# Optimization experiments

Hardware: AMD Instinct MI355X
Metric: run time of the kernel (lower is better)

Reference implementation:

```python
import jax, jax.numpy as jnp
import numpy as np

N_NODES = 20000
N_EDGES = 320000
NFEAT = 50
ALPHA = 0.2  # leaky relu slope
EPS = 1e-16


def _gat_head(x, src, dst, W, a, concat):
    # x: (N, Fin), W: (Fin, Fout), a: (2*Fout,)
    N = x.shape[0]
    Wh = x @ W                      # (N, Fout)
    Fout = W.shape[1]
    # edge_h @ a == Wh[src] @ a[:Fout] + Wh[dst] @ a[Fout:]
    s_src = Wh @ a[:Fout]           # (N,)
    s_dst = Wh @ a[Fout:]           # (N,)
    e = jax.nn.leaky_relu(s_src[src] + s_dst[dst], negative_slope=ALPHA)  # (E,)
    # segment softmax over incoming edges of each target node
    e_max = jax.ops.segment_max(e, dst, num_segments=N)   # (N,)
    e_exp = jnp.exp(e - e_max[dst])                         # (E,)
    e_sum = jax.ops.segment_sum(e_exp, dst, num_segments=N)
    att = e_exp / (e_sum[dst] + EPS)                        # (E,)
    msg = Wh[src] * att[:, None]                            # (E, Fout)
    h = jax.ops.segment_sum(msg, dst, num_segments=N)       # (N, Fout)
    return jax.nn.elu(h) if concat else h


def _multi_head(x, src, dst, W, a, concat):
    # W: (H, Fin, Fout), a: (H, 2*Fout) -> (H, N, Fout)
    return jax.vmap(_gat_head, in_axes=(None, None, None, 0, 0, None))(x, src, dst, W, a, concat)


def setup_inputs() -> dict:
    key = jax.random.key(0)
    ks = jax.random.split(key, 8)
    x = jax.random.normal(ks[0], (N_NODES, NFEAT), dtype=jnp.float32)
    edge_index = jax.random.randint(ks[1], (2, N_EDGES), 0, N_NODES, dtype=jnp.int64)
    s = 0.1
    W1 = jax.random.normal(ks[2], (4, NFEAT, 256), dtype=jnp.float32) * s
    a1 = jax.random.normal(ks[3], (4, 512), dtype=jnp.float32) * s
    W2 = jax.random.normal(ks[4], (4, 1024, 256), dtype=jnp.float32) * s
    a2 = jax.random.normal(ks[5], (4, 512), dtype=jnp.float32) * s
    W3 = jax.random.normal(ks[6], (6, 1024, 121), dtype=jnp.float32) * s
    a3 = jax.random.normal(ks[7], (6, 242), dtype=jnp.float32) * s
    return {"x": x, "edge_index": edge_index, "W1": W1, "a1": a1, "W2": W2, "a2": a2, "W3": W3, "a3": a3}


def reference(x, edge_index, W1, a1, W2, a2, W3, a3):
    src, dst = edge_index[0], edge_index[1]
    N = x.shape[0]
    # layer 1: 4 heads, concat -> (N, 1024), then elu
    h1 = _multi_head(x, src, dst, W1, a1, True)      # (4, N, 256)
    x1 = jnp.transpose(h1, (1, 0, 2)).reshape(N, -1)  # concat along feature dim
    x1 = jax.nn.elu(x1)
    # layer 2: 4 heads, concat + skip connection, then elu
    h2 = _multi_head(x1, src, dst, W2, a2, True)
    x2 = jnp.transpose(h2, (1, 0, 2)).reshape(N, -1)
    x2 = jax.nn.elu(x2 + x1)
    # layer 3: 6 heads, no concat-elu, mean over heads
    h3 = _multi_head(x2, src, dst, W3, a3, False)     # (6, N, 121)
    x3 = jnp.mean(h3, axis=0)
    return jax.nn.sigmoid(x3)
```

## Files before the change

kernel.cpp:

```cpp
#include <hip/hip_runtime.h>
#include <cstdint>

#define N_NODES 20000
#define N_EDGES 320000
#define ALPHA 0.2f
#define GAT_EPS 1e-16f
#define MPAD 20096
#define RBLK 157
#define RHI 20
#define SCAN_BLKS 80
#define BT_ROWS 1152

typedef __attribute__((ext_vector_type(8))) _Float16 half8;
typedef __attribute__((ext_vector_type(4))) _Float16 half4t;
typedef __attribute__((ext_vector_type(16))) float f32x16;
typedef __attribute__((ext_vector_type(2))) float f32x2;

__device__ __forceinline__ float elu1(float x) { return x > 0.f ? x : __expf(x) - 1.f; }

__device__ __forceinline__ unsigned char f2fp8(float x) {
    return (unsigned char)(__builtin_amdgcn_cvt_pk_fp8_f32(x, 0.f, 0, false) & 0xff);
}

__device__ __forceinline__ void async16(const void* g, void* l) {
    __builtin_amdgcn_global_load_lds(
        (const __attribute__((address_space(1))) unsigned int*)g,
        (__attribute__((address_space(3))) unsigned int*)l, 16, 0, 0);
}

__device__ __forceinline__ float rdlanef(float v, int j) {
    return __int_as_float(__builtin_amdgcn_readlane(__float_as_int(v), j));
}

__global__ void hist_kernel(const int* __restrict__ dst, int* __restrict__ counts, int E) {
    int e = blockIdx.x * blockDim.x + threadIdx.x;
    if (e < E) atomicAdd(&counts[dst[e]], 1);
}

__global__ void scan1_kernel(const int* __restrict__ counts, int* __restrict__ excl,
                             int* __restrict__ partial, int N) {
    __shared__ int sh[256];
    int t = threadIdx.x, b = blockIdx.x;
    int i = b * 256 + t;
    int v = (i < N) ? counts[i] : 0;
    sh[t] = v;
    __syncthreads();
    for (int d = 1; d < 256; d <<= 1) {
        int x = (t >= d) ? sh[t - d] : 0;
        __syncthreads();
        sh[t] += x;
        __syncthreads();
    }
    if (i < N) excl[i] = sh[t] - v;
    if (t == 255) partial[b] = sh[255];
}

__global__ void scan2_kernel(int* __restrict__ partial) {
    __shared__ int sh[128];
    int t = threadIdx.x;
    int v = (t < SCAN_BLKS) ? partial[t] : 0;
    sh[t] = v;
    __syncthreads();
    for (int d = 1; d < 128; d <<= 1) {
        int x = (t >= d) ? sh[t - d] : 0;
        __syncthreads();
        sh[t] += x;
        __syncthreads();
    }
    if (t < SCAN_BLKS) partial[t] = sh[t] - v;
}

__global__ void scan3_kernel(const int* __restrict__ excl, const int* __restrict__ partial,
                             int* __restrict__ rowptr, int* __restrict__ cursor, int N, int E) {
    int t = threadIdx.x, b = blockIdx.x;
    int i = b * 256 + t;
    if (i < N) {
        int v = excl[i] + partial[b];
        rowptr[i] = v;
        cursor[i] = v;
    }
    if (i == 0) rowptr[N] = E;
}

__global__ void scatter_kernel(const int* __restrict__ src, const int* __restrict__ dst,
                               int* __restrict__ cursor, int* __restrict__ esrc, int E) {
    int e = blockIdx.x * blockDim.x + threadIdx.x;
    if (e < E) {
        int p = atomicAdd(&cursor[dst[e]], 1);
        esrc[p] = src[e];
    }
}

__global__ void pack_x16(const float* __restrict__ x, _Float16* __restrict__ A) {
    int idx = blockIdx.x * 256 + threadIdx.x;
    int r = idx >> 6, c = idx & 63;
    float v = (r < N_NODES && c < 50) ? x[r * 50 + c] : 0.f;
    A[idx] = (_Float16)v;
}

__global__ void pack_bt1(const float* __restrict__ W, _Float16* __restrict__ Bt) {
    int idx = blockIdx.x * 256 + threadIdx.x;
    int c = idx >> 6, k = idx & 63;
    int h = c >> 8, f = c & 255;
    float v = (k < 50) ? W[((size_t)h * 50 + k) * 256 + f] : 0.f;
    Bt[idx] = (_Float16)v;
}

__global__ void pack_bt16(const float* __restrict__ W, _Float16* __restrict__ Bt,
                          int F, int Fpad, int Ctot) {
    int c = blockIdx.y;
    int k = blockIdx.x * blockDim.x + threadIdx.x;
    float v = 0.f;
    if (c < Ctot) {
        int h = c / Fpad, f = c - h * Fpad;
        if (f < F) v = W[(size_t)h * 1024 * F + (size_t)k * F + f];
    }
    Bt[(size_t)c * 1024 + k] = (_Float16)v;
}

__global__ __launch_bounds__(64) void wtilde_kernel(const float* __restrict__ W,
                                                    const float* __restrict__ a,
                                                    _Float16* __restrict__ BT, int Kreal,
                                                    int Kdim, int F, int H, int Nfeat) {
    int k = blockIdx.x, j = blockIdx.y;
    if (j >= 2 * H) return;
    int lane = threadIdx.x;
    int h = j < H ? j : j - H;
    int ao = j < H ? 0 : F;
    float s = 0.f;
    if (k < Kreal) {
        const float* wp = W + ((size_t)h * Kreal + k) * F;
        const float* ap = a + (size_t)h * 2 * F + ao;
        for (int f = lane; f < F; f += 64) s += wp[f] * ap[f];
    }
#pragma unroll
    for (int off = 32; off; off >>= 1) s += __shfl_down(s, off);
    if (lane == 0) BT[(size_t)(Nfeat + j) * Kdim + k] = (_Float16)s;
}

__global__ __launch_bounds__(256) void gemm_f16(const _Float16* __restrict__ A,
                                                const _Float16* __restrict__ BT,
                                                unsigned char* __restrict__ C8,
                                                float* __restrict__ SPRE,
                                                int M, int Nfeat, int ld, int Kdim, int Cblk) {
    int id = blockIdx.x;
    int xm = id & 7, q = id >> 3;
    int cb = q % Cblk, rh = q / Cblk;
    int rb = rh * 8 + xm;
    if (rb >= RBLK) return;
    __shared__ __align__(16) _Float16 sA[2][128 * 64];
    __shared__ __align__(16) _Float16 sB[2][128 * 64];
    int t = threadIdx.x;
    int row0 = rb * 128, col0 = cb * 128;
    int lane = t & 63, wave = t >> 6;
    int wm = wave >> 1, wn = wave & 1;
    int l31 = lane & 31;
    int lhi = lane >> 5;

    const _Float16* gA = A + (size_t)row0 * Kdim;
    const _Float16* gB = BT + (size_t)col0 * Kdim;

    int sR[4], sgl[4];
#pragma unroll
    for (int i = 0; i < 4; i++) {
        int m = i * 256 + t;
        sR[i] = m >> 3;
        sgl[i] = (m & 7) ^ (sR[i] & 7);
    }

    f32x16 acc[2][2] = {};

#pragma unroll
    for (int i = 0; i < 4; i++) {
        const _Float16* pa = gA + (size_t)sR[i] * Kdim + sgl[i] * 8;
        const _Float16* pb = gB + (size_t)sR[i] * Kdim + sgl[i] * 8;
        async16(pa, &sA[0][(i * 256 + t) * 8]);
        async16(pb, &sB[0][(i * 256 + t) * 8]);
    }

    int cur = 0;
    for (int k0 = 0; k0 < Kdim; k0 += 64) {
        __syncthreads();
        int nxt = k0 + 64;
        if (nxt < Kdim) {
            int nb = cur ^ 1;
#pragma unroll
            for (int i = 0; i < 4; i++) {
                const _Float16* pa = gA + (size_t)sR[i] * Kdim + nxt + sgl[i] * 8;
                const _Float16* pb = gB + (size_t)sR[i] * Kdim + nxt + sgl[i] * 8;
                async16(pa, &sA[nb][(i * 256 + t) * 8]);
                async16(pb, &sB[nb][(i * 256 + t) * 8]);
            }
        }
        const _Float16* cA = sA[cur];
        const _Float16* cB = sB[cur];
#pragma unroll
        for (int kk = 0; kk < 4; kk++) {
            int g = kk * 2 + lhi;
            half8 af[2], bf[2];
#pragma unroll
            for (int mt = 0; mt < 2; mt++) {
                int R = wm * 64 + mt * 32 + l31;
                int gp = g ^ (R & 7);
                af[mt] = *(const half8*)(cA + R * 64 + gp * 8);
            }
#pragma unroll
            for (int nt = 0; nt < 2; nt++) {
                int R = wn * 64 + nt * 32 + l31;
                int gp = g ^ (R & 7);
                bf[nt] = *(const half8*)(cB + R * 64 + gp * 8);
            }
#pragma unroll
            for (int mt = 0; mt < 2; mt++)
#pragma unroll
                for (int nt = 0; nt < 2; nt++)
                    acc[mt][nt] = __builtin_amdgcn_mfma_f32_32x32x16_f16(af[mt], bf[nt], acc[mt][nt], 0, 0, 0);
        }
        cur ^= 1;
    }

    int cb32 = col0 + wn * 64 + l31;
    int rb32 = row0 + wm * 64 + 4 * lhi;
#pragma unroll
    for (int mt = 0; mt < 2; mt++)
#pragma unroll
        for (int nt = 0; nt < 2; nt++) {
            int gc = cb32 + nt * 32;
            if (gc < Nfeat) {
#pragma unroll
                for (int r = 0; r < 16; r++) {
                    int gr = rb32 + mt * 32 + (r & 3) + 8 * (r >> 2);
                    if (gr < M) C8[(size_t)gr * ld + gc] = f2fp8(acc[mt][nt][r]);
                }
            } else if (gc < Nfeat + 12) {
                int j = gc - Nfeat;
#pragma unroll
                for (int r = 0; r < 16; r++) {
                    int gr = rb32 + mt * 32 + (r & 3) + 8 * (r >> 2);
                    if (gr < M) SPRE[(size_t)j * N_NODES + gr] = acc[mt][nt][r];
                }
            }
        }
}

__global__ __launch_bounds__(256) void attagg256_kernel(const int* __restrict__ rowptr,
                                                        const int* __restrict__ esrc,
                                                        const float* __restrict__ SPRE,
                                                        const unsigned char* __restrict__ WH8,
                                                        _Float16* __restrict__ X16,
                                                        int use_skip, int N) {
    int n = blockIdx.x;
    int h = threadIdx.x >> 6;
    int lane = threadIdx.x & 63;
    int start = rowptr[n], end = rowptr[n + 1];
    const float* ss = SPRE + (size_t)h * N;
    float sd = SPRE[(size_t)(4 + h) * N + n];

    float m = -1e30f, s = 0.f;
    int sidx = 0; float ssc = -1e30f;
    for (int e0 = start; e0 < end; e0 += 64) {
        int e = e0 + lane;
        bool act = e < end;
        int idx = act ? esrc[e] : 0;
        float sc = -1e30f;
        if (act) {
            sc = ss[idx] + sd;
            sc = sc > 0.f ? sc : ALPHA * sc;
        }
        sidx = idx; ssc = sc;
        float mn = fmaxf(m, sc);
        s = s * __expf(m - mn) + (act ? __expf(sc - mn) : 0.f);
        m = mn;
    }
#pragma unroll
    for (int off = 1; off < 64; off <<= 1) {
        float mo = __shfl_xor(m, off);
        float so = __shfl_xor(s, off);
        float mn = fmaxf(m, mo);
        s = s * __expf(m - mn) + so * __expf(mo - mn);
        m = mn;
    }
    float inv = 1.f / (s + GAT_EPS);

    const unsigned char* Wb = WH8 + h * 256 + lane * 4;
    float a0 = 0.f, a1 = 0.f, a2 = 0.f, a3 = 0.f;
    int lastStart = start + (((end - start - 1) >> 6) << 6);
    for (int e0 = start; e0 < end; e0 += 64) {
        int e = e0 + lane;
        bool act = e < end;
        int idx; float sc;
        if (e0 == lastStart) { idx = sidx; sc = ssc; }
        else {
            idx = act ? esrc[e] : 0;
            sc = -1e30f;
            if (act) {
                sc = ss[idx] + sd;
                sc = sc > 0.f ? sc : ALPHA * sc;
            }
        }
        float p = act ? __expf(sc - m) * inv : 0.f;
        int cnt = end - e0; if (cnt > 64) cnt = 64;
        int j = 0;
        for (; j + 4 <= cnt; j += 4) {
            int i0 = __builtin_amdgcn_readlane(idx, j);
            int i1 = __builtin_amdgcn_readlane(idx, j + 1);
            int i2 = __builtin_amdgcn_readlane(idx, j + 2);
            int i3 = __builtin_amdgcn_readlane(idx, j + 3);
            float p0 = rdlanef(p, j), p1 = rdlanef(p, j + 1);
            float p2 = rdlanef(p, j + 2), p3 = rdlanef(p, j + 3);
            unsigned int w0 = *(const unsigned int*)(Wb + (size_t)i0 * 1024);
            unsigned int w1 = *(const unsigned int*)(Wb + (size_t)i1 * 1024);
            unsigned int w2 = *(const unsigned int*)(Wb + (size_t)i2 * 1024);
            unsigned int w3 = *(const unsigned int*)(Wb + (size_t)i3 * 1024);
            f32x2 l0 = __builtin_amdgcn_cvt_pk_f32_fp8((int)w0, false);
            f32x2 h0v = __builtin_amdgcn_cvt_pk_f32_fp8((int)w0, true);
            f32x2 l1 = __builtin_amdgcn_cvt_pk_f32_fp8((int)w1, false);
            f32x2 h1v = __builtin_amdgcn_cvt_pk_f32_fp8((int)w1, true);
            f32x2 l2 = __builtin_amdgcn_cvt_pk_f32_fp8((int)w2, false);
            f32x2 h2v = __builtin_amdgcn_cvt_pk_f32_fp8((int)w2, true);
            f32x2 l3 = __builtin_amdgcn_cvt_pk_f32_fp8((int)w3, false);
            f32x2 h3v = __builtin_amdgcn_cvt_pk_f32_fp8((int)w3, true);
            a0 += p0 * l0.x + p1 * l1.x + p2 * l2.x + p3 * l3.x;
            a1 += p0 * l0.y + p1 * l1.y + p2 * l2.y + p3 * l3.y;
            a2 += p0 * h0v.x + p1 * h1v.x + p2 * h2v.x + p3 * h3v.x;
            a3 += p0 * h0v.y + p1 * h1v.y + p2 * h2v.y + p3 * h3v.y;
        }
        for (; j < cnt; j++) {
            int ij = __builtin_amdgcn_readlane(idx, j);
            float pj = rdlanef(p, j);
            unsigned int w = *(const unsigned int*)(Wb + (size_t)ij * 1024);
            f32x2 lo = __builtin_amdgcn_cvt_pk_f32_fp8((int)w, false);
            f32x2 hi = __builtin_amdgcn_cvt_pk_f32_fp8((int)w, true);
            a0 += pj * lo.x; a1 += pj * lo.y; a2 += pj * hi.x; a3 += pj * hi.y;
        }
    }

    size_t o = (size_t)n * 1024 + h * 256 + lane * 4;
    float v0, v1, v2, v3;
    if (use_skip) {
        half4t sk = *(const half4t*)(X16 + o);
        v0 = elu1(elu1(a0) + (float)sk.x);
        v1 = elu1(elu1(a1) + (float)sk.y);
        v2 = elu1(elu1(a2) + (float)sk.z);
        v3 = elu1(elu1(a3) + (float)sk.w);
    } else {
        v0 = elu1(elu1(a0)); v1 = elu1(elu1(a1));
        v2 = elu1(elu1(a2)); v3 = elu1(elu1(a3));
    }
    half4t r;
    r.x = (_Float16)v0; r.y = (_Float16)v1; r.z = (_Float16)v2; r.w = (_Float16)v3;
    *(half4t*)(X16 + o) = r;
}

__global__ __launch_bounds__(384) void attagg726_kernel(const int* __restrict__ rowptr,
                                                        const int* __restrict__ esrc,
                                                        const float* __restrict__ SPRE,
                                                        const unsigned char* __restrict__ WH8,
                                                        float* __restrict__ out, int N) {
    __shared__ float part[6][124];
    int n = blockIdx.x;
    int t = threadIdx.x;
    int h = t >> 6;
    int lane = t & 63;
    int start = rowptr[n], end = rowptr[n + 1];
    const float* ss = SPRE + (size_t)h * N;
    float sd = SPRE[(size_t)(6 + h) * N + n];

    float m = -1e30f, s = 0.f;
    int sidx = 0; float ssc = -1e30f;
    for (int e0 = start; e0 < end; e0 += 64) {
        int e = e0 + lane;
        bool act = e < end;
        int idx = act ? esrc[e] : 0;
        float sc = -1e30f;
        if (act) {
            sc = ss[idx] + sd;
            sc = sc > 0.f ? sc : ALPHA * sc;
        }
        sidx = idx; ssc = sc;
        float mn = fmaxf(m, sc);
        s = s * __expf(m - mn) + (act ? __expf(sc - mn) : 0.f);
        m = mn;
    }
#pragma unroll
    for (int off = 1; off < 64; off <<= 1) {
        float mo = __shfl_xor(m, off);
        float so = __shfl_xor(s, off);
        float mn = fmaxf(m, mo);
        s = s * __expf(m - mn) + so * __expf(mo - mn);
        m = mn;
    }
    float inv = 1.f / (s + GAT_EPS);

    const unsigned char* Wb = WH8 + h * 124 + 2 * lane;
    float a0 = 0.f, a1 = 0.f;
    int lastStart = start + (((end - start - 1) >> 6) << 6);
    for (int e0 = start; e0 < end; e0 += 64) {
        int e = e0 + lane;
        bool act = e < end;
        int idx; float sc;
        if (e0 == lastStart) { idx = sidx; sc = ssc; }
        else {
            idx = act ? esrc[e] : 0;
            sc = -1e30f;
            if (act) {
                sc = ss[idx] + sd;
                sc = sc > 0.f ? sc : ALPHA * sc;
            }
        }
        float p = act ? __expf(sc - m) * inv : 0.f;
        int cnt = end - e0; if (cnt > 64) cnt = 64;
        int j = 0;
        for (; j + 4 <= cnt; j += 4) {
            int i0 = __builtin_amdgcn_readlane(idx, j);
            int i1 = __builtin_amdgcn_readlane(idx, j + 1);
            int i2 = __builtin_amdgcn_readlane(idx, j + 2);
            int i3 = __builtin_amdgcn_readlane(idx, j + 3);
            float p0 = rdlanef(p, j), p1 = rdlanef(p, j + 1);
            float p2 = rdlanef(p, j + 2), p3 = rdlanef(p, j + 3);
            unsigned short w0 = *(const unsigned short*)(Wb + (size_t)i0 * 768);
            unsigned short w1 = *(const unsigned short*)(Wb + (size_t)i1 * 768);
            unsigned short w2 = *(const unsigned short*)(Wb + (size_t)i2 * 768);
            unsigned short w3 = *(const unsigned short*)(Wb + (size_t)i3 * 768);
            f32x2 f0 = __builtin_amdgcn_cvt_pk_f32_fp8((int)w0, false);
            f32x2 f1 = __builtin_amdgcn_cvt_pk_f32_fp8((int)w1, false);
            f32x2 f2 = __builtin_amdgcn_cvt_pk_f32_fp8((int)w2, false);
            f32x2 f3 = __builtin_amdgcn_cvt_pk_f32_fp8((int)w3, false);
            a0 += p0 * f0.x + p1 * f1.x + p2 * f2.x + p3 * f3.x;
            a1 += p0 * f0.y + p1 * f1.y + p2 * f2.y + p3 * f3.y;
        }
        for (; j < cnt; j++) {
            int ij = __builtin_amdgcn_readlane(idx, j);
            float pj = rdlanef(p, j);
            unsigned short w = *(const unsigned short*)(Wb + (size_t)ij * 768);
            f32x2 f = __builtin_amdgcn_cvt_pk_f32_fp8((int)w, false);
            a0 += pj * f.x; a1 += pj * f.y;
        }
    }
    if (lane < 62) {
        part[h][2 * lane]     = a0;
        part[h][2 * lane + 1] = a1;
    }
    __syncthreads();
    if (t < 121) {
        float tot = (part[0][t] + part[1][t] + part[2][t] +
                     part[3][t] + part[4][t] + part[5][t]) * (1.f / 6.f);
        out[(size_t)n * 121 + t] = 1.f / (1.f + __expf(-tot));
    }
}

extern "C" void kernel_launch(void* const* d_in, const int* in_sizes, int n_in,
                              void* d_out, int out_size, void* d_ws, size_t ws_size,
                              hipStream_t stream) {
    const float* x  = (const float*)d_in[0];
    const int*   ei = (const int*)d_in[1];
    const float* W1 = (const float*)d_in[2];
    const float* a1 = (const float*)d_in[3];
    const float* W2 = (const float*)d_in[4];
    const float* a2 = (const float*)d_in[5];
    const float* W3 = (const float*)d_in[6];
    const float* a3 = (const float*)d_in[7];
    float* out = (float*)d_out;
    const int N = N_NODES, E = N_EDGES;
    const int* src = ei;
    const int* dst = ei + E;

    char* ws = (char*)d_ws;
    size_t off = 0;
    auto alloc = [&](size_t b) { size_t o = off; off += (b + 255) & ~(size_t)255; return o; };
    _Float16* X16  = (_Float16*)(ws + alloc((size_t)MPAD * 1024 * 2));
    unsigned char* WH8 = (unsigned char*)(ws + alloc((size_t)MPAD * 1024));
    _Float16* BT16 = (_Float16*)(ws + alloc((size_t)BT_ROWS * 1024 * 2));
    _Float16* A1   = (_Float16*)(ws + alloc((size_t)MPAD * 64 * 2));
    _Float16* BT1  = (_Float16*)(ws + alloc((size_t)BT_ROWS * 64 * 2));
    float* SPRE   = (float*)(ws + alloc((size_t)12 * N * 4));
    int*   rowptr = (int*)(ws + alloc((size_t)(N + 1) * 4));
    int*   cursor = (int*)(ws + alloc((size_t)N * 4));
    int*   counts = (int*)(ws + alloc((size_t)N * 4));
    int*   excl   = (int*)(ws + alloc((size_t)N * 4));
    int*   partial= (int*)(ws + alloc((size_t)SCAN_BLKS * 4));
    int*   esrc   = (int*)(ws + alloc((size_t)E * 4));

    hipMemsetAsync(counts, 0, (size_t)N * 4, stream);
    hist_kernel<<<(E + 255) / 256, 256, 0, stream>>>(dst, counts, E);
    scan1_kernel<<<SCAN_BLKS, 256, 0, stream>>>(counts, excl, partial, N);
    scan2_kernel<<<1, 128, 0, stream>>>(partial);
    scan3_kernel<<<SCAN_BLKS, 256, 0, stream>>>(excl, partial, rowptr, cursor, N, E);
    scatter_kernel<<<(E + 255) / 256, 256, 0, stream>>>(src, dst, cursor, esrc, E);
    hipMemsetAsync(X16 + (size_t)N * 1024, 0, (size_t)(MPAD - N) * 1024 * 2, stream);

    pack_x16<<<MPAD * 64 / 256, 256, 0, stream>>>(x, A1);
    pack_bt1<<<1024 * 64 / 256, 256, 0, stream>>>(W1, BT1);
    wtilde_kernel<<<dim3(64, 8), 64, 0, stream>>>(W1, a1, BT1, 50, 64, 256, 4, 1024);
    gemm_f16<<<8 * RHI * 9, 256, 0, stream>>>(A1, BT1, WH8, SPRE, N, 1024, 1024, 64, 9);
    attagg256_kernel<<<N, 256, 0, stream>>>(rowptr, esrc, SPRE, WH8, X16, 0, N);

    pack_bt16<<<dim3(4, 1024), 256, 0, stream>>>(W2, BT16, 256, 256, 1024);
    wtilde_kernel<<<dim3(1024, 8), 64, 0, stream>>>(W2, a2, BT16, 1024, 1024, 256, 4, 1024);
    gemm_f16<<<8 * RHI * 9, 256, 0, stream>>>(X16, BT16, WH8, SPRE, N, 1024, 1024, 1024, 9);
    attagg256_kernel<<<N, 256, 0, stream>>>(rowptr, esrc, SPRE, WH8, X16, 1, N);

    pack_bt16<<<dim3(4, 744), 256, 0, stream>>>(W3, BT16, 121, 124, 744);
    wtilde_kernel<<<dim3(1024, 12), 64, 0, stream>>>(W3, a3, BT16, 1024, 1024, 121, 6, 744);
    gemm_f16<<<8 * RHI * 6, 256, 0, stream>>>(X16, BT16, WH8, SPRE, N, 744, 768, 1024, 6);
    attagg726_kernel<<<N, 384, 0, stream>>>(rowptr, esrc, SPRE, WH8, out, N);
}
```

Before: 462.5 us.

## Gather full 1KB edge rows with 16-byte loads split across waves via LDS

The attention-aggregation kernels no longer give each wave one head that reads 4 or 2 bytes per lane per edge. Each wave now takes every 4th or 6th edge and reads the whole fp8 row with one 16-byte load per lane, accumulating through packed FMAs. Per-edge probabilities and indices are shared through LDS, and the partial sums are reduced across waves in shared memory at the end. Layer 3 is padded to 128 columns per head so its rows are 768 bytes and aligned, and the score columns are placed inside the padding so the GEMM emits them there. This trades extra barriers and an LDS reduction for wider, better-coalesced gathers and one software-prefetched load in flight per wave.

```diff
diff --git a/kernel.cpp b/kernel.cpp
--- a/kernel.cpp
+++ b/kernel.cpp
@@ -28,8 +28,15 @@
         (__attribute__((address_space(3))) unsigned int*)l, 16, 0, 0);
 }
 
-__device__ __forceinline__ float rdlanef(float v, int j) {
-    return __int_as_float(__builtin_amdgcn_readlane(__float_as_int(v), j));
+__device__ __forceinline__ f32x2 pkfma(f32x2 a, f32x2 b, f32x2 c) {
+    f32x2 d;
+    asm("v_pk_fma_f32 %0, %1, %2, %3" : "=v"(d) : "v"(a), "v"(b), "v"(c));
+    return d;
+}
+
+template <bool HI>
+__device__ __forceinline__ f32x2 cvt8(unsigned int u) {
+    return __builtin_amdgcn_cvt_pk_f32_fp8((int)u, HI);
 }
 
 __global__ void hist_kernel(const int* __restrict__ dst, int* __restrict__ counts, int E) {
@@ -121,7 +128,8 @@
 __global__ __launch_bounds__(64) void wtilde_kernel(const float* __restrict__ W,
                                                     const float* __restrict__ a,
                                                     _Float16* __restrict__ BT, int Kreal,
-                                                    int Kdim, int F, int H, int Nfeat) {
+                                                    int Kdim, int F, int H, int Nfeat,
+                                                    int padmode) {
     int k = blockIdx.x, j = blockIdx.y;
     if (j >= 2 * H) return;
     int lane = threadIdx.x;
@@ -135,14 +143,18 @@
     }
 #pragma unroll
     for (int off = 32; off; off >>= 1) s += __shfl_down(s, off);
-    if (lane == 0) BT[(size_t)(Nfeat + j) * Kdim + k] = (_Float16)s;
+    if (lane == 0) {
+        int row = padmode ? (h * 128 + 121 + (j >= H ? 1 : 0)) : (Nfeat + j);
+        BT[(size_t)row * Kdim + k] = (_Float16)s;
+    }
 }
 
 __global__ __launch_bounds__(256) void gemm_f16(const _Float16* __restrict__ A,
                                                 const _Float16* __restrict__ BT,
                                                 unsigned char* __restrict__ C8,
                                                 float* __restrict__ SPRE,
-                                                int M, int Nfeat, int ld, int Kdim, int Cblk) {
+                                                int M, int Nfeat, int ld, int Kdim, int Cblk,
+                                                int l3pad) {
     int id = blockIdx.x;
     int xm = id & 7, q = id >> 3;
     int cb = q % Cblk, rh = q / Cblk;
@@ -227,12 +239,18 @@
         for (int nt = 0; nt < 2; nt++) {
             int gc = cb32 + nt * 32;
             if (gc < Nfeat) {
+                int fr = gc & 127;
+                int sj = (fr - 121) * 6 + (gc >> 7);
+                bool sp = l3pad && (fr == 121 || fr == 122);
 #pragma unroll
                 for (int r = 0; r < 16; r++) {
                     int gr = rb32 + mt * 32 + (r & 3) + 8 * (r >> 2);
-                    if (gr < M) C8[(size_t)gr * ld + gc] = f2fp8(acc[mt][nt][r]);
+                    if (gr < M) {
+                        C8[(size_t)gr * ld + gc] = f2fp8(acc[mt][nt][r]);
+                        if (sp) SPRE[(size_t)sj * N_NODES + gr] = acc[mt][nt][r];
+                    }
                 }
-            } else if (gc < Nfeat + 12) {
+            } else if (!l3pad && gc < Nfeat + 12) {
                 int j = gc - Nfeat;
 #pragma unroll
                 for (int r = 0; r < 16; r++) {
@@ -249,12 +267,16 @@
                                                         const unsigned char* __restrict__ WH8,
                                                         _Float16* __restrict__ X16,
                                                         int use_skip, int N) {
+    __shared__ float part[4 * 1024];
+    __shared__ float Pp[4][72];
+    __shared__ int Ii[64];
     int n = blockIdx.x;
-    int h = threadIdx.x >> 6;
-    int lane = threadIdx.x & 63;
+    int t = threadIdx.x;
+    int wv = t >> 6;
+    int lane = t & 63;
     int start = rowptr[n], end = rowptr[n + 1];
-    const float* ss = SPRE + (size_t)h * N;
-    float sd = SPRE[(size_t)(4 + h) * N + n];
+    const float* ss = SPRE + (size_t)wv * N;
+    float sd = SPRE[(size_t)(4 + wv) * N + n];
 
     float m = -1e30f, s = 0.f;
     int sidx = 0; float ssc = -1e30f;
@@ -282,8 +304,9 @@
     }
     float inv = 1.f / (s + GAT_EPS);
 
-    const unsigned char* Wb = WH8 + h * 256 + lane * 4;
-    float a0 = 0.f, a1 = 0.f, a2 = 0.f, a3 = 0.f;
+    int hf = lane >> 4;
+    const unsigned char* Wb = WH8 + lane * 16;
+    f32x2 acc[8] = {};
     int lastStart = start + (((end - start - 1) >> 6) << 6);
     for (int e0 = start; e0 < end; e0 += 64) {
         int e = e0 + lane;
@@ -299,43 +322,54 @@
             }
         }
         float p = act ? __expf(sc - m) * inv : 0.f;
+        __syncthreads();
+        Pp[wv][lane] = p;
+        if (wv == 0) Ii[lane] = idx;
+        __syncthreads();
         int cnt = end - e0; if (cnt > 64) cnt = 64;
-        int j = 0;
-        for (; j + 4 <= cnt; j += 4) {
-            int i0 = __builtin_amdgcn_readlane(idx, j);
-            int i1 = __builtin_amdgcn_readlane(idx, j + 1);
-            int i2 = __builtin_amdgcn_readlane(idx, j + 2);
-            int i3 = __builtin_amdgcn_readlane(idx, j + 3);
-            float p0 = rdlanef(p, j), p1 = rdlanef(p, j + 1);
-            float p2 = rdlanef(p, j + 2), p3 = rdlanef(p, j + 3);
-            unsigned int w0 = *(const unsigned int*)(Wb + (size_t)i0 * 1024);
-            unsigned int w1 = *(const unsigned int*)(Wb + (size_t)i1 * 1024);
-            unsigned int w2 = *(const unsigned int*)(Wb + (size_t)i2 * 1024);
-            unsigned int w3 = *(const unsigned int*)(Wb + (size_t)i3 * 1024);
-            f32x2 l0 = __builtin_amdgcn_cvt_pk_f32_fp8((int)w0, false);
-            f32x2 h0v = __builtin_amdgcn_cvt_pk_f32_fp8((int)w0, true);
-            f32x2 l1 = __builtin_amdgcn_cvt_pk_f32_fp8((int)w1, false);
-            f32x2 h1v = __builtin_amdgcn_cvt_pk_f32_fp8((int)w1, true);
-            f32x2 l2 = __builtin_amdgcn_cvt_pk_f32_fp8((int)w2, false);
-            f32x2 h2v = __builtin_amdgcn_cvt_pk_f32_fp8((int)w2, true);
-            f32x2 l3 = __builtin_amdgcn_cvt_pk_f32_fp8((int)w3, false);
-            f32x2 h3v = __builtin_amdgcn_cvt_pk_f32_fp8((int)w3, true);
-            a0 += p0 * l0.x + p1 * l1.x + p2 * l2.x + p3 * l3.x;
-            a1 += p0 * l0.y + p1 * l1.y + p2 * l2.y + p3 * l3.y;
-            a2 += p0 * h0v.x + p1 * h1v.x + p2 * h2v.x + p3 * h3v.x;
-            a3 += p0 * h0v.y + p1 * h1v.y + p2 * h2v.y + p3 * h3v.y;
-        }
-        for (; j < cnt; j++) {
-            int ij = __builtin_amdgcn_readlane(idx, j);
-            float pj = rdlanef(p, j);
-            unsigned int w = *(const unsigned int*)(Wb + (size_t)ij * 1024);
-            f32x2 lo = __builtin_amdgcn_cvt_pk_f32_fp8((int)w, false);
-            f32x2 hi = __builtin_amdgcn_cvt_pk_f32_fp8((int)w, true);
-            a0 += pj * lo.x; a1 += pj * lo.y; a2 += pj * hi.x; a3 += pj * hi.y;
-        }
-    }
-
-    size_t o = (size_t)n * 1024 + h * 256 + lane * 4;
+        int j = wv;
+        if (j < cnt) {
+            int ij = Ii[j];
+            float pj = Pp[hf][j];
+            uint4 w = *(const uint4*)(Wb + ((size_t)(unsigned)ij << 10));
+            for (;;) {
+                int j2 = j + 4;
+                bool more = j2 < cnt;
+                int ij2 = 0; float pj2 = 0.f; uint4 w2;
+                if (more) {
+                    ij2 = Ii[j2];
+                    pj2 = Pp[hf][j2];
+                    w2 = *(const uint4*)(Wb + ((size_t)(unsigned)ij2 << 10));
+                }
+                f32x2 pv; pv.x = pj; pv.y = pj;
+                acc[0] = pkfma(cvt8<false>(w.x), pv, acc[0]);
+                acc[1] = pkfma(cvt8<true>(w.x),  pv, acc[1]);
+                acc[2] = pkfma(cvt8<false>(w.y), pv, acc[2]);
+                acc[3] = pkfma(cvt8<true>(w.y),  pv, acc[3]);
+                acc[4] = pkfma(cvt8<false>(w.z), pv, acc[4]);
+                acc[5] = pkfma(cvt8<true>(w.z),  pv, acc[5]);
+                acc[6] = pkfma(cvt8<false>(w.w), pv, acc[6]);
+                acc[7] = pkfma(cvt8<true>(w.w),  pv, acc[7]);
+                if (!more) break;
+                j = j2; pj = pj2; w = w2;
+            }
+        }
+    }
+
+#pragma unroll
+    for (int k = 0; k < 8; k++)
+        *(f32x2*)&part[wv * 1024 + lane * 16 + 2 * k] = acc[k];
+    __syncthreads();
+    int f0 = t * 4;
+    float4 q0 = *(const float4*)&part[f0];
+    float4 q1 = *(const float4*)&part[1024 + f0];
+    float4 q2 = *(const float4*)&part[2048 + f0];
+    float4 q3 = *(const float4*)&part[3072 + f0];
+    float a0 = q0.x + q1.x + q2.x + q3.x;
+    float a1 = q0.y + q1.y + q2.y + q3.y;
+    float a2 = q0.z + q1.z + q2.z + q3.z;
+    float a3 = q0.w + q1.w + q2.w + q3.w;
+    size_t o = (size_t)n * 1024 + f0;
     float v0, v1, v2, v3;
     if (use_skip) {
         half4t sk = *(const half4t*)(X16 + o);
@@ -357,14 +391,16 @@
                                                         const float* __restrict__ SPRE,
                                                         const unsigned char* __restrict__ WH8,
                                                         float* __restrict__ out, int N) {
-    __shared__ float part[6][124];
+    __shared__ float part[6 * 768];
+    __shared__ float Pp[6][72];
+    __shared__ int Ii[64];
     int n = blockIdx.x;
     int t = threadIdx.x;
-    int h = t >> 6;
+    int wv = t >> 6;
     int lane = t & 63;
     int start = rowptr[n], end = rowptr[n + 1];
-    const float* ss = SPRE + (size_t)h * N;
-    float sd = SPRE[(size_t)(6 + h) * N + n];
+    const float* ss = SPRE + (size_t)wv * N;
+    float sd = SPRE[(size_t)(6 + wv) * N + n];
 
     float m = -1e30f, s = 0.f;
     int sidx = 0; float ssc = -1e30f;
@@ -392,8 +428,9 @@
     }
     float inv = 1.f / (s + GAT_EPS);
 
-    const unsigned char* Wb = WH8 + h * 124 + 2 * lane;
-    float a0 = 0.f, a1 = 0.f;
+    int hf = (lane < 48) ? (lane >> 3) : 0;
+    const unsigned char* Wb = WH8 + lane * 16;
+    f32x2 acc[8] = {};
     int lastStart = start + (((end - start - 1) >> 6) << 6);
     for (int e0 = start; e0 < end; e0 += 64) {
         int e = e0 + lane;
@@ -409,42 +446,58 @@
             }
         }
         float p = act ? __expf(sc - m) * inv : 0.f;
+        __syncthreads();
+        Pp[wv][lane] = p;
+        if (wv == 0) Ii[lane] = idx;
+        __syncthreads();
         int cnt = end - e0; if (cnt > 64) cnt = 64;
-        int j = 0;
-        for (; j + 4 <= cnt; j += 4) {
-            int i0 = __builtin_amdgcn_readlane(idx, j);
-            int i1 = __builtin_amdgcn_readlane(idx, j + 1);
-            int i2 = __builtin_amdgcn_readlane(idx, j + 2);
-            int i3 = __builtin_amdgcn_readlane(idx, j + 3);
-            float p0 = rdlanef(p, j), p1 = rdlanef(p, j + 1);
-            float p2 = rdlanef(p, j + 2), p3 = rdlanef(p, j + 3);
-            unsigned short w0 = *(const unsigned short*)(Wb + (size_t)i0 * 768);
-            unsigned short w1 = *(const unsigned short*)(Wb + (size_t)i1 * 768);
-            unsigned short w2 = *(const unsigned short*)(Wb + (size_t)i2 * 768);
-            unsigned short w3 = *(const unsigned short*)(Wb + (size_t)i3 * 768);
-            f32x2 f0 = __builtin_amdgcn_cvt_pk_f32_fp8((int)w0, false);
-            f32x2 f1 = __builtin_amdgcn_cvt_pk_f32_fp8((int)w1, false);
-            f32x2 f2 = __builtin_amdgcn_cvt_pk_f32_fp8((int)w2, false);
-            f32x2 f3 = __builtin_amdgcn_cvt_pk_f32_fp8((int)w3, false);
-            a0 += p0 * f0.x + p1 * f1.x + p2 * f2.x + p3 * f3.x;
-            a1 += p0 * f0.y + p1 * f1.y + p2 * f2.y + p3 * f3.y;
-        }
-        for (; j < cnt; j++) {
-            int ij = __builtin_amdgcn_readlane(idx, j);
-            float pj = rdlanef(p, j);
-            unsigned short w = *(const unsigned short*)(Wb + (size_t)ij * 768);
-            f32x2 f = __builtin_amdgcn_cvt_pk_f32_fp8((int)w, false);
-            a0 += pj * f.x; a1 += pj * f.y;
-        }
-    }
-    if (lane < 62) {
-        part[h][2 * lane]     = a0;
-        part[h][2 * lane + 1] = a1;
+        int j = wv;
+        if (j < cnt) {
+            int ij = Ii[j];
+            float pj = Pp[hf][j];
+            uint4 w = *(const uint4*)(Wb + (size_t)(unsigned)ij * 768u);
+            for (;;) {
+                int j2 = j + 6;
+                bool more = j2 < cnt;
+                int ij2 = 0; float pj2 = 0.f; uint4 w2;
+                if (more) {
+                    ij2 = Ii[j2];
+                    pj2 = Pp[hf][j2];
+                    w2 = *(const uint4*)(Wb + (size_t)(unsigned)ij2 * 768u);
+                }
+                f32x2 pv; pv.x = pj; pv.y = pj;
+                acc[0] = pkfma(cvt8<false>(w.x), pv, acc[0]);
+                acc[1] = pkfma(cvt8<true>(w.x),  pv, acc[1]);
+                acc[2] = pkfma(cvt8<false>(w.y), pv, acc[2]);
+                acc[3] = pkfma(cvt8<true>(w.y),  pv, acc[3]);
+                acc[4] = pkfma(cvt8<false>(w.z), pv, acc[4]);
+                acc[5] = pkfma(cvt8<true>(w.z),  pv, acc[5]);
+                acc[6] = pkfma(cvt8<false>(w.w), pv, acc[6]);
+                acc[7] = pkfma(cvt8<true>(w.w),  pv, acc[7]);
+                if (!more) break;
+                j = j2; pj = pj2; w = w2;
+            }
+        }
+    }
+
+    if (lane < 48) {
+#pragma unroll
+        for (int k = 0; k < 8; k++)
+            *(f32x2*)&part[wv * 768 + lane * 16 + 2 * k] = acc[k];
+    }
+    __syncthreads();
+    for (int f = t; f < 768; f += 384) {
+        float sx = 0.f;
+#pragma unroll
+        for (int w6 = 0; w6 < 6; w6++) sx += part[w6 * 768 + f];
+        part[f] = sx;
     }
     __syncthreads();
     if (t < 121) {
-        float tot = (part[0][t] + part[1][t] + part[2][t] +
-                     part[3][t] + part[4][t] + part[5][t]) * (1.f / 6.f);
+        float tot = 0.f;
+#pragma unroll
+        for (int hh = 0; hh < 6; hh++) tot += part[hh * 128 + t];
+        tot *= (1.f / 6.f);
         out[(size_t)n * 121 + t] = 1.f / (1.f + __expf(-tot));
     }
 }
@@ -491,17 +544,17 @@
 
     pack_x16<<<MPAD * 64 / 256, 256, 0, stream>>>(x, A1);
     pack_bt1<<<1024 * 64 / 256, 256, 0, stream>>>(W1, BT1);
-    wtilde_kernel<<<dim3(64, 8), 64, 0, stream>>>(W1, a1, BT1, 50, 64, 256, 4, 1024);
-    gemm_f16<<<8 * RHI * 9, 256, 0, stream>>>(A1, BT1, WH8, SPRE, N, 1024, 1024, 64, 9);
+    wtilde_kernel<<<dim3(64, 8), 64, 0, stream>>>(W1, a1, BT1, 50, 64, 256, 4, 1024, 0);
+    gemm_f16<<<8 * RHI * 9, 256, 0, stream>>>(A1, BT1, WH8, SPRE, N, 1024, 1024, 64, 9, 0);
     attagg256_kernel<<<N, 256, 0, stream>>>(rowptr, esrc, SPRE, WH8, X16, 0, N);
 
     pack_bt16<<<dim3(4, 1024), 256, 0, stream>>>(W2, BT16, 256, 256, 1024);
-    wtilde_kernel<<<dim3(1024, 8), 64, 0, stream>>>(W2, a2, BT16, 1024, 1024, 256, 4, 1024);
-    gemm_f16<<<8 * RHI * 9, 256, 0, stream>>>(X16, BT16, WH8, SPRE, N, 1024, 1024, 1024, 9);
+    wtilde_kernel<<<dim3(1024, 8), 64, 0, stream>>>(W2, a2, BT16, 1024, 1024, 256, 4, 1024, 0);
+    gemm_f16<<<8 * RHI * 9, 256, 0, stream>>>(X16, BT16, WH8, SPRE, N, 1024, 1024, 1024, 9, 0);
     attagg256_kernel<<<N, 256, 0, stream>>>(rowptr, esrc, SPRE, WH8, X16, 1, N);
 
-    pack_bt16<<<dim3(4, 744), 256, 0, stream>>>(W3, BT16, 121, 124, 744);
-    wtilde_kernel<<<dim3(1024, 12), 64, 0, stream>>>(W3, a3, BT16, 1024, 1024, 121, 6, 744);
-    gemm_f16<<<8 * RHI * 6, 256, 0, stream>>>(X16, BT16, WH8, SPRE, N, 744, 768, 1024, 6);
+    pack_bt16<<<dim3(4, 768), 256, 0, stream>>>(W3, BT16, 121, 128, 768);
+    wtilde_kernel<<<dim3(1024, 12), 64, 0, stream>>>(W3, a3, BT16, 1024, 1024, 121, 6, 768, 1);
+    gemm_f16<<<8 * RHI * 6, 256, 0, stream>>>(X16, BT16, WH8, SPRE, N, 768, 768, 1024, 6, 1);
     attagg726_kernel<<<N, 384, 0, stream>>>(rowptr, esrc, SPRE, WH8, out, N);
 }
```

After: 464.9 us. About the same (+0.5%).
